# Performance work log

Hardware: AMD Instinct MI355X
Metric: run time of the kernel (lower is better)

## Reference

```python
import jax, jax.numpy as jnp
import numpy as np


def soft_threshold24(w):
    """2:4 soft thresholding along the last dim (groups of 4):
    keep top-2 magnitudes per group, subtract the 2nd-smallest magnitude
    (largest pruned value) from kept elements: sign(w)*relu(|w|-t)."""
    shape = w.shape
    g = w.reshape(-1, 4)
    mag = jnp.abs(g)
    s = jnp.sort(mag, axis=-1)          # ascending: [s0,s1,s2,s3]
    t = s[:, 1:2]                        # threshold = 2nd smallest magnitude
    out = jnp.sign(g) * jnp.maximum(mag - t, 0.0)
    return out.reshape(shape)


def fp8_mm(a, b):
    # fake_fp8_mm: cast operands to fp16, accumulate in fp32
    return jnp.matmul(a.astype(jnp.float16), b.astype(jnp.float16),
                      preferred_element_type=jnp.float32)


def _init_scale(w):
    ws = soft_threshold24(w)
    return jnp.sum(w * ws) / jnp.sum(ws * ws)


def setup_inputs() -> dict:
    key = jax.random.key(0)
    k1, k2, k3 = jax.random.split(key, 3)
    in_f, out_f, rank = 4096, 4096, 64
    B, S = 4, 2048
    x = jax.random.normal(k1, (B, S, in_f), dtype=jnp.float32)
    # kaiming_uniform_(a=sqrt(5)) -> U(-1/sqrt(fan_in), 1/sqrt(fan_in))
    b_in = 1.0 / np.sqrt(in_f)
    b_out = 1.0 / np.sqrt(rank)
    weight_in = jax.random.uniform(k2, (rank, in_f), minval=-b_in, maxval=b_in, dtype=jnp.float32)
    weight_out = jax.random.uniform(k3, (out_f, rank), minval=-b_out, maxval=b_out, dtype=jnp.float32)
    bias = jnp.zeros((out_f,), dtype=jnp.float32)
    scale_in = _init_scale(weight_in).astype(jnp.float32)
    scale_out = _init_scale(weight_out).astype(jnp.float32)
    return {"x": x, "weight_in": weight_in, "weight_out": weight_out,
            "bias": bias, "scale_in": scale_in, "scale_out": scale_out}


def reference(x, weight_in, weight_out, bias, scale_in, scale_out):
    rank = weight_in.shape[0]
    scaling = 1.0 / rank  # alpha / rank, alpha = 1.0
    sw_in = soft_threshold24(weight_in) * scale_in    # (rank, in_f)
    sw_out = soft_threshold24(weight_out) * scale_out  # (out_f, rank)
    B, S, in_f = x.shape
    xp = fp8_mm(x.reshape(-1, in_f), sw_in.T)          # (B*S, rank) fp32
    out = fp8_mm(xp, sw_out.T) + bias                   # (B*S, out_f)
    return out.reshape(B, S, -1) * scaling
```

## Files before the change

### kernel.cpp

```cpp
#include <hip/hip_runtime.h>

typedef _Float16 half8 __attribute__((ext_vector_type(8)));
typedef float f32x4 __attribute__((ext_vector_type(4)));

#define IN_F 4096
#define OUT_F 4096
#define RANK 64
#define M_TOT 8192
#define KCHUNK 1024
#define NKC (IN_F / KCHUNK)
#define KC2 512
#define NKC2 (IN_F / KC2)
#define NBLK (M_TOT / 16)

__device__ __forceinline__ half8 thresh8(const float* __restrict__ p, float scale) {
    half8 h;
    #pragma unroll
    for (int g = 0; g < 2; ++g) {
        f32x4 v = *(const f32x4*)(p + 4 * g);
        float m0 = fabsf(v[0]), m1 = fabsf(v[1]), m2 = fabsf(v[2]), m3 = fabsf(v[3]);
        float lo1 = fminf(m0, m1), hi1 = fmaxf(m0, m1);
        float lo2 = fminf(m2, m3), hi2 = fmaxf(m2, m3);
        float t = fminf(fmaxf(lo1, lo2), fminf(hi1, hi2));
        h[4 * g + 0] = (_Float16)(copysignf(fmaxf(m0 - t, 0.0f), v[0]) * scale);
        h[4 * g + 1] = (_Float16)(copysignf(fmaxf(m1 - t, 0.0f), v[1]) * scale);
        h[4 * g + 2] = (_Float16)(copysignf(fmaxf(m2 - t, 0.0f), v[2]) * scale);
        h[4 * g + 3] = (_Float16)(copysignf(fmaxf(m3 - t, 0.0f), v[3]) * scale);
    }
    return h;
}

__global__ __launch_bounds__(256) void prep_kernel(
    const float* __restrict__ w_in, const float* __restrict__ w_out,
    const float* __restrict__ s_in_p, const float* __restrict__ s_out_p,
    _Float16* __restrict__ sw_in, _Float16* __restrict__ sw_out)
{
    const int tid = blockIdx.x * 256 + threadIdx.x;
    const int HALF = RANK * IN_F / 8;
    const float* src; _Float16* dst; float sc; int g;
    if (tid < HALF) { src = w_in;  dst = sw_in;  sc = *s_in_p;  g = tid; }
    else            { src = w_out; dst = sw_out; sc = *s_out_p; g = tid - HALF; }
    half8 h = thresh8(src + (size_t)g * 8, sc);
    *(half8*)(dst + (size_t)g * 8) = h;
}

__global__ __launch_bounds__(256) void k_p1b(
    const float* __restrict__ x, const _Float16* __restrict__ sw_in,
    _Float16* __restrict__ xpw)
{
    __shared__ _Float16 xh[2][16][KC2];
    __shared__ _Float16 xpl[16][RANK];

    const int t    = threadIdx.x;
    const int wave = t >> 6;
    const int lane = t & 63;
    const int row  = lane & 15;
    const int kg   = lane >> 4;
    const int m0   = blockIdx.x * 16;
    const int sr   = wave;
    const int skb  = lane;

    f32x4 ra[4], rb[4];
    auto issue = [&](int kc) {
        #pragma unroll
        for (int i = 0; i < 4; ++i) {
            const float* src = x + (size_t)(m0 + i * 4 + sr) * IN_F + kc + skb * 8;
            ra[i] = *(const f32x4*)src;
            rb[i] = *(const f32x4*)(src + 4);
        }
    };
    auto cstore = [&](int buf) {
        #pragma unroll
        for (int i = 0; i < 4; ++i) {
            const int r = i * 4 + sr;
            half8 h;
            #pragma unroll
            for (int j = 0; j < 4; ++j) {
                h[j]     = (_Float16)ra[i][j];
                h[j + 4] = (_Float16)rb[i][j];
            }
            *(half8*)&xh[buf][r][(skb ^ (r & 7)) << 3] = h;
        }
    };

    const _Float16* wr = sw_in + (size_t)(wave * 16 + row) * IN_F + kg * 8;
    f32x4 acc1 = {0.f, 0.f, 0.f, 0.f};

    issue(0);
    cstore(0);
    __syncthreads();
    int cur = 0;
    #pragma unroll 1
    for (int kci = 0; kci < NKC2; ++kci) {
        if (kci + 1 < NKC2) issue((kci + 1) * KC2);
        const int kc = kci * KC2;
        #pragma unroll
        for (int k0 = 0; k0 < KC2; k0 += 64) {
            const int kb = (k0 >> 3) + kg;
            half8 alo = *(const half8*)&xh[cur][row][(kb       ^ (row & 7)) << 3];
            half8 ahi = *(const half8*)&xh[cur][row][((kb + 4) ^ (row & 7)) << 3];
            half8 blo = *(const half8*)(wr + kc + k0);
            half8 bhi = *(const half8*)(wr + kc + k0 + 32);
            acc1 = __builtin_amdgcn_mfma_f32_16x16x32_f16(alo, blo, acc1, 0, 0, 0);
            acc1 = __builtin_amdgcn_mfma_f32_16x16x32_f16(ahi, bhi, acc1, 0, 0, 0);
        }
        if (kci + 1 < NKC2) cstore(cur ^ 1);
        __syncthreads();
        cur ^= 1;
    }

    #pragma unroll
    for (int r = 0; r < 4; ++r)
        xpl[kg * 4 + r][wave * 16 + row] = (_Float16)acc1[r];
    __syncthreads();

    for (int i = t; i < 16 * RANK; i += 256)
        xpw[(size_t)blockIdx.x * 1024 + i] = xpl[i >> 6][i & 63];
}

__global__ __launch_bounds__(256) void k_p2(
    const _Float16* __restrict__ xpw, const _Float16* __restrict__ sw_out,
    const float* __restrict__ bias, float* __restrict__ out)
{
    __shared__ __align__(16) char smem[2 * 16 * KCHUNK * 2];
    __shared__ _Float16 xpl[16][RANK];

    const int t    = threadIdx.x;
    const int wave = t >> 6;
    const int lane = t & 63;
    const int row  = lane & 15;
    const int kg   = lane >> 4;
    const int m0   = blockIdx.x * 16;

    for (int i = t; i < 16 * RANK; i += 256)
        xpl[i >> 6][i & 63] = xpw[(size_t)blockIdx.x * 1024 + i];
    __syncthreads();

    const half8 a_lo = *(const half8*)&xpl[row][kg * 8];
    const half8 a_hi = *(const half8*)&xpl[row][kg * 8 + 32];
    const float scaling = 1.0f / 64.0f;

    float* tb = (float*)smem + wave * 2048;
    const int ncol0 = wave * 1024;

    for (int g = 0; g < 8; ++g) {
        const int gc = ncol0 + g * 128;
        #pragma unroll
        for (int c2 = 0; c2 < 2; ++c2) {
            const int cg = gc + c2 * 64;
            f32x4 acc[4] = {{0.f,0.f,0.f,0.f},{0.f,0.f,0.f,0.f},
                            {0.f,0.f,0.f,0.f},{0.f,0.f,0.f,0.f}};
            #pragma unroll
            for (int nt = 0; nt < 4; ++nt) {
                const _Float16* wp = sw_out + (size_t)(cg + nt * 16 + row) * RANK + kg * 8;
                half8 blo = *(const half8*)wp;
                half8 bhi = *(const half8*)(wp + 32);
                acc[nt] = __builtin_amdgcn_mfma_f32_16x16x32_f16(a_lo, blo, acc[nt], 0, 0, 0);
                acc[nt] = __builtin_amdgcn_mfma_f32_16x16x32_f16(a_hi, bhi, acc[nt], 0, 0, 0);
            }
            #pragma unroll
            for (int nt = 0; nt < 4; ++nt) {
                const float b = bias[cg + nt * 16 + row];
                #pragma unroll
                for (int r = 0; r < 4; ++r)
                    tb[(kg * 4 + r) * 128 + c2 * 64 + nt * 16 + row] =
                        (acc[nt][r] + b) * scaling;
            }
        }
        #pragma unroll
        for (int i = 0; i < 8; ++i) {
            const int s    = i * 64 + lane;
            const int orow = s >> 5;
            const int c4   = s & 31;
            f32x4 v = *(const f32x4*)&tb[orow * 128 + c4 * 4];
            *(f32x4*)&out[(size_t)(m0 + orow) * OUT_F + gc + c4 * 4] = v;
        }
    }
}

__global__ __launch_bounds__(256) void k_full(
    const float* __restrict__ x, const _Float16* __restrict__ sw_in,
    const _Float16* __restrict__ sw_out, const float* __restrict__ bias,
    float* __restrict__ out)
{
    __shared__ __align__(16) char smem[2 * 16 * KCHUNK * 2];
    __shared__ _Float16 xpl[16][RANK];
    auto xh = (_Float16 (*)[16][KCHUNK])smem;

    const int t    = threadIdx.x;
    const int wave = t >> 6;
    const int lane = t & 63;
    const int row  = lane & 15;
    const int kg   = lane >> 4;
    const int m0   = blockIdx.x * 16;
    const int sr   = t >> 7;
    const int skb  = t & 127;

    f32x4 ra[8], rb[8];
    auto issue = [&](int kc) {
        #pragma unroll
        for (int i = 0; i < 8; ++i) {
            const float* src = x + (size_t)(m0 + i * 2 + sr) * IN_F + kc + skb * 8;
            ra[i] = *(const f32x4*)src;
            rb[i] = *(const f32x4*)(src + 4);
        }
    };
    auto cstore = [&](int buf) {
        #pragma unroll
        for (int i = 0; i < 8; ++i) {
            const int r = i * 2 + sr;
            half8 h;
            #pragma unroll
            for (int j = 0; j < 4; ++j) {
                h[j]     = (_Float16)ra[i][j];
                h[j + 4] = (_Float16)rb[i][j];
            }
            *(half8*)&xh[buf][r][(skb ^ (r & 7)) << 3] = h;
        }
    };

    const _Float16* wr = sw_in + (size_t)(wave * 16 + row) * IN_F + kg * 8;
    f32x4 acc1 = {0.f, 0.f, 0.f, 0.f};

    issue(0);
    cstore(0);
    __syncthreads();
    int cur = 0;
    for (int kci = 0; kci < NKC; ++kci) {
        if (kci + 1 < NKC) issue((kci + 1) * KCHUNK);
        const int kc = kci * KCHUNK;
        #pragma unroll 4
        for (int k0 = 0; k0 < KCHUNK; k0 += 64) {
            const int kb = (k0 >> 3) + kg;
            half8 alo = *(const half8*)&xh[cur][row][(kb       ^ (row & 7)) << 3];
            half8 ahi = *(const half8*)&xh[cur][row][((kb + 4) ^ (row & 7)) << 3];
            half8 blo = *(const half8*)(wr + kc + k0);
            half8 bhi = *(const half8*)(wr + kc + k0 + 32);
            acc1 = __builtin_amdgcn_mfma_f32_16x16x32_f16(alo, blo, acc1, 0, 0, 0);
            acc1 = __builtin_amdgcn_mfma_f32_16x16x32_f16(ahi, bhi, acc1, 0, 0, 0);
        }
        if (kci + 1 < NKC) cstore(cur ^ 1);
        __syncthreads();
        cur ^= 1;
    }

    #pragma unroll
    for (int r = 0; r < 4; ++r)
        xpl[kg * 4 + r][wave * 16 + row] = (_Float16)acc1[r];
    __syncthreads();

    const half8 a_lo = *(const half8*)&xpl[row][kg * 8];
    const half8 a_hi = *(const half8*)&xpl[row][kg * 8 + 32];
    const float scaling = 1.0f / 64.0f;

    float* tb = (float*)smem + wave * 2048;
    const int ncol0 = wave * 1024;

    for (int g = 0; g < 8; ++g) {
        const int gc = ncol0 + g * 128;
        #pragma unroll
        for (int c2 = 0; c2 < 2; ++c2) {
            const int cg = gc + c2 * 64;
            f32x4 acc[4] = {{0.f,0.f,0.f,0.f},{0.f,0.f,0.f,0.f},
                            {0.f,0.f,0.f,0.f},{0.f,0.f,0.f,0.f}};
            #pragma unroll
            for (int nt = 0; nt < 4; ++nt) {
                const _Float16* wp = sw_out + (size_t)(cg + nt * 16 + row) * RANK + kg * 8;
                half8 blo = *(const half8*)wp;
                half8 bhi = *(const half8*)(wp + 32);
                acc[nt] = __builtin_amdgcn_mfma_f32_16x16x32_f16(a_lo, blo, acc[nt], 0, 0, 0);
                acc[nt] = __builtin_amdgcn_mfma_f32_16x16x32_f16(a_hi, bhi, acc[nt], 0, 0, 0);
            }
            #pragma unroll
            for (int nt = 0; nt < 4; ++nt) {
                const float b = bias[cg + nt * 16 + row];
                #pragma unroll
                for (int r = 0; r < 4; ++r)
                    tb[(kg * 4 + r) * 128 + c2 * 64 + nt * 16 + row] =
                        (acc[nt][r] + b) * scaling;
            }
        }
        #pragma unroll
        for (int i = 0; i < 8; ++i) {
            const int s    = i * 64 + lane;
            const int orow = s >> 5;
            const int c4   = s & 31;
            f32x4 v = *(const f32x4*)&tb[orow * 128 + c4 * 4];
            *(f32x4*)&out[(size_t)(m0 + orow) * OUT_F + gc + c4 * 4] = v;
        }
    }
}

__global__ __launch_bounds__(256) void loro_fallback(
    const float* __restrict__ x, const float* __restrict__ w_in,
    const float* __restrict__ w_out, const float* __restrict__ bias,
    const float* __restrict__ s_in_p, const float* __restrict__ s_out_p,
    float* __restrict__ out)
{
    __shared__ _Float16 xh[16][KCHUNK];
    __shared__ _Float16 xpl[16][RANK];

    const int t    = threadIdx.x;
    const int wave = t >> 6;
    const int lane = t & 63;
    const int row  = lane & 15;
    const int kg   = lane >> 4;
    const int m0   = blockIdx.x * 16;
    const float s_in  = *s_in_p;
    const float s_out = *s_out_p;

    f32x4 acc1 = {0.f, 0.f, 0.f, 0.f};
    const float* wr = w_in + (size_t)(wave * 16 + row) * IN_F + kg * 8;

    for (int kc = 0; kc < IN_F; kc += KCHUNK) {
        __syncthreads();
        #pragma unroll
        for (int i = 0; i < 8; ++i) {
            const int f  = i * 2048 + t * 8;
            const int r  = f >> 10;
            const int cl = f & (KCHUNK - 1);
            const float* src = x + (size_t)(m0 + r) * IN_F + kc + cl;
            f32x4 a = *(const f32x4*)src;
            f32x4 b = *(const f32x4*)(src + 4);
            #pragma unroll
            for (int j = 0; j < 4; ++j) {
                xh[r][cl + j]     = (_Float16)a[j];
                xh[r][cl + 4 + j] = (_Float16)b[j];
            }
        }
        __syncthreads();

        #pragma unroll 4
        for (int k0 = 0; k0 < KCHUNK; k0 += 64) {
            half8 alo = *(const half8*)&xh[row][k0 + kg * 8];
            half8 ahi = *(const half8*)&xh[row][k0 + kg * 8 + 32];
            half8 blo = thresh8(wr + kc + k0,      s_in);
            half8 bhi = thresh8(wr + kc + k0 + 32, s_in);
            acc1 = __builtin_amdgcn_mfma_f32_16x16x32_f16(alo, blo, acc1, 0, 0, 0);
            acc1 = __builtin_amdgcn_mfma_f32_16x16x32_f16(ahi, bhi, acc1, 0, 0, 0);
        }
    }

    #pragma unroll
    for (int r = 0; r < 4; ++r)
        xpl[kg * 4 + r][wave * 16 + row] = (_Float16)acc1[r];
    __syncthreads();

    const half8 a_lo = *(const half8*)&xpl[row][kg * 8];
    const half8 a_hi = *(const half8*)&xpl[row][kg * 8 + 32];
    const float scaling = 1.0f / 64.0f;

    for (int c = 0; c < 16; ++c) {
        f32x4 acc[4] = {{0.f,0.f,0.f,0.f},{0.f,0.f,0.f,0.f},
                        {0.f,0.f,0.f,0.f},{0.f,0.f,0.f,0.f}};
        #pragma unroll
        for (int nt = 0; nt < 4; ++nt) {
            const float* wp = w_out
                + (size_t)(c * 256 + wave * 64 + nt * 16 + row) * RANK + kg * 8;
            half8 blo = thresh8(wp,      s_out);
            half8 bhi = thresh8(wp + 32, s_out);
            acc[nt] = __builtin_amdgcn_mfma_f32_16x16x32_f16(a_lo, blo, acc[nt], 0, 0, 0);
            acc[nt] = __builtin_amdgcn_mfma_f32_16x16x32_f16(a_hi, bhi, acc[nt], 0, 0, 0);
        }
        #pragma unroll
        for (int nt = 0; nt < 4; ++nt) {
            const int col = c * 256 + wave * 64 + nt * 16 + row;
            const float b = bias[col];
            #pragma unroll
            for (int r = 0; r < 4; ++r)
                out[(size_t)(m0 + kg * 4 + r) * OUT_F + col] = (acc[nt][r] + b) * scaling;
        }
    }
}

extern "C" void kernel_launch(void* const* d_in, const int* in_sizes, int n_in,
                              void* d_out, int out_size, void* d_ws, size_t ws_size,
                              hipStream_t stream) {
    (void)in_sizes; (void)n_in; (void)out_size;
    const float* x     = (const float*)d_in[0];
    const float* w_in  = (const float*)d_in[1];
    const float* w_out = (const float*)d_in[2];
    const float* bias  = (const float*)d_in[3];
    const float* s_in  = (const float*)d_in[4];
    const float* s_out = (const float*)d_in[5];
    float* out = (float*)d_out;

    const size_t need_sw   = (size_t)(RANK * IN_F + OUT_F * RANK) * sizeof(_Float16);
    const size_t need_full = need_sw + (size_t)NBLK * 1024 * sizeof(_Float16);

    if (d_ws != nullptr && ws_size >= need_full) {
        _Float16* sw_in  = (_Float16*)d_ws;
        _Float16* sw_out = sw_in + (size_t)RANK * IN_F;
        _Float16* xpw    = (_Float16*)((char*)d_ws + need_sw);

        prep_kernel<<<(RANK * IN_F + OUT_F * RANK) / 8 / 256, 256, 0, stream>>>(
            w_in, w_out, s_in, s_out, sw_in, sw_out);
        k_p1b<<<NBLK, 256, 0, stream>>>(x, sw_in, xpw);
        k_p2 <<<NBLK, 256, 0, stream>>>(xpw, sw_out, bias, out);
    } else if (d_ws != nullptr && ws_size >= need_sw) {
        _Float16* sw_in  = (_Float16*)d_ws;
        _Float16* sw_out = sw_in + (size_t)RANK * IN_F;
        prep_kernel<<<(RANK * IN_F + OUT_F * RANK) / 8 / 256, 256, 0, stream>>>(
            w_in, w_out, s_in, s_out, sw_in, sw_out);
        k_full<<<NBLK, 256, 0, stream>>>(x, sw_in, sw_out, bias, out);
    } else {
        loro_fallback<<<M_TOT / 16, 256, 0, stream>>>(
            x, w_in, w_out, bias, s_in, s_out, out);
    }
}
```

Baseline: 103.1 us.

## Stage x via direct global-to-LDS loads and split K across two wave groups

Replaces the register-staged fp32-to-fp16 conversion of x in the first GEMM with direct global_load_lds transfers of raw fp32 into a swizzled LDS double buffer, converting to fp16 only when reading fragments. Block size grows to 512 threads, with two wave groups alternating K chunks and combining their partial results through an LDS reduction before writing xp. The aim is to hide global load latency without tying up registers and to give more waves per block for latency hiding. In exchange, LDS use doubles because data is stored as fp32, and half the waves sit idle in each chunk iteration.

```diff
diff --git a/kernel.cpp b/kernel.cpp
--- a/kernel.cpp
+++ b/kernel.cpp
@@ -9,8 +9,6 @@
 #define M_TOT 8192
 #define KCHUNK 1024
 #define NKC (IN_F / KCHUNK)
-#define KC2 512
-#define NKC2 (IN_F / KC2)
 #define NBLK (M_TOT / 16)
 
 __device__ __forceinline__ half8 thresh8(const float* __restrict__ p, float scale) {
@@ -44,78 +42,83 @@
     *(half8*)(dst + (size_t)g * 8) = h;
 }
 
-__global__ __launch_bounds__(256) void k_p1b(
+__global__ __launch_bounds__(512) void k_p1g(
     const float* __restrict__ x, const _Float16* __restrict__ sw_in,
     _Float16* __restrict__ xpw)
 {
-    __shared__ _Float16 xh[2][16][KC2];
-    __shared__ _Float16 xpl[16][RANK];
+    __shared__ float xf[2][16][512];
+    __shared__ float red[2][16][RANK];
 
     const int t    = threadIdx.x;
     const int wave = t >> 6;
     const int lane = t & 63;
     const int row  = lane & 15;
     const int kg   = lane >> 4;
+    const int kh   = wave >> 2;
+    const int ng   = wave & 3;
     const int m0   = blockIdx.x * 16;
-    const int sr   = wave;
-    const int skb  = lane;
-
-    f32x4 ra[4], rb[4];
-    auto issue = [&](int kc) {
-        #pragma unroll
-        for (int i = 0; i < 4; ++i) {
-            const float* src = x + (size_t)(m0 + i * 4 + sr) * IN_F + kc + skb * 8;
-            ra[i] = *(const f32x4*)src;
-            rb[i] = *(const f32x4*)(src + 4);
+    const int rs   = row & 7;
+
+    auto stage = [&](int buf, int kc) {
+        #pragma unroll
+        for (int j = 0; j < 4; ++j) {
+            const int s  = wave * 4 + j;
+            const int r  = s >> 1;
+            const int b  = (s & 1) * 64 + lane;
+            const int gb = b ^ (r & 7);
+            const float* g = x + (size_t)(m0 + r) * IN_F + kc + gb * 4;
+            void* l = (void*)&xf[buf][r][(s & 1) * 256];
+            __builtin_amdgcn_global_load_lds(
+                (const __attribute__((address_space(1))) void*)g,
+                (__attribute__((address_space(3))) void*)l, 16, 0, 0);
         }
     };
-    auto cstore = [&](int buf) {
-        #pragma unroll
-        for (int i = 0; i < 4; ++i) {
-            const int r = i * 4 + sr;
-            half8 h;
-            #pragma unroll
-            for (int j = 0; j < 4; ++j) {
-                h[j]     = (_Float16)ra[i][j];
-                h[j + 4] = (_Float16)rb[i][j];
-            }
-            *(half8*)&xh[buf][r][(skb ^ (r & 7)) << 3] = h;
-        }
-    };
-
-    const _Float16* wr = sw_in + (size_t)(wave * 16 + row) * IN_F + kg * 8;
+
+    const _Float16* wr = sw_in + (size_t)(ng * 16 + row) * IN_F + kg * 8;
     f32x4 acc1 = {0.f, 0.f, 0.f, 0.f};
 
-    issue(0);
-    cstore(0);
+    stage(0, 0);
     __syncthreads();
     int cur = 0;
     #pragma unroll 1
-    for (int kci = 0; kci < NKC2; ++kci) {
-        if (kci + 1 < NKC2) issue((kci + 1) * KC2);
-        const int kc = kci * KC2;
-        #pragma unroll
-        for (int k0 = 0; k0 < KC2; k0 += 64) {
-            const int kb = (k0 >> 3) + kg;
-            half8 alo = *(const half8*)&xh[cur][row][(kb       ^ (row & 7)) << 3];
-            half8 ahi = *(const half8*)&xh[cur][row][((kb + 4) ^ (row & 7)) << 3];
-            half8 blo = *(const half8*)(wr + kc + k0);
-            half8 bhi = *(const half8*)(wr + kc + k0 + 32);
-            acc1 = __builtin_amdgcn_mfma_f32_16x16x32_f16(alo, blo, acc1, 0, 0, 0);
-            acc1 = __builtin_amdgcn_mfma_f32_16x16x32_f16(ahi, bhi, acc1, 0, 0, 0);
-        }
-        if (kci + 1 < NKC2) cstore(cur ^ 1);
+    for (int kci = 0; kci < 8; ++kci) {
+        if (kci + 1 < 8) stage(cur ^ 1, (kci + 1) * 512);
+        if ((kci & 1) == kh) {
+            const int kc = kci * 512;
+            #pragma unroll
+            for (int k0 = 0; k0 < 512; k0 += 64) {
+                const int g0 = (k0 >> 2) + kg * 2;
+                const float* base = &xf[cur][row][0];
+                f32x4 a0 = *(const f32x4*)(base + (((g0    ) ^ rs) << 2));
+                f32x4 a1 = *(const f32x4*)(base + (((g0 + 1) ^ rs) << 2));
+                f32x4 a2 = *(const f32x4*)(base + (((g0 + 8) ^ rs) << 2));
+                f32x4 a3 = *(const f32x4*)(base + (((g0 + 9) ^ rs) << 2));
+                half8 alo, ahi;
+                #pragma unroll
+                for (int i = 0; i < 4; ++i) {
+                    alo[i]     = (_Float16)a0[i];
+                    alo[i + 4] = (_Float16)a1[i];
+                    ahi[i]     = (_Float16)a2[i];
+                    ahi[i + 4] = (_Float16)a3[i];
+                }
+                half8 blo = *(const half8*)(wr + kc + k0);
+                half8 bhi = *(const half8*)(wr + kc + k0 + 32);
+                acc1 = __builtin_amdgcn_mfma_f32_16x16x32_f16(alo, blo, acc1, 0, 0, 0);
+                acc1 = __builtin_amdgcn_mfma_f32_16x16x32_f16(ahi, bhi, acc1, 0, 0, 0);
+            }
+        }
         __syncthreads();
         cur ^= 1;
     }
 
     #pragma unroll
     for (int r = 0; r < 4; ++r)
-        xpl[kg * 4 + r][wave * 16 + row] = (_Float16)acc1[r];
-    __syncthreads();
-
-    for (int i = t; i < 16 * RANK; i += 256)
-        xpw[(size_t)blockIdx.x * 1024 + i] = xpl[i >> 6][i & 63];
+        red[kh][kg * 4 + r][ng * 16 + row] = acc1[r];
+    __syncthreads();
+
+    for (int i = t; i < 16 * RANK; i += 512)
+        xpw[(size_t)blockIdx.x * 1024 + i] =
+            (_Float16)(red[0][i >> 6][i & 63] + red[1][i >> 6][i & 63]);
 }
 
 __global__ __launch_bounds__(256) void k_p2(
@@ -395,7 +398,7 @@
 
         prep_kernel<<<(RANK * IN_F + OUT_F * RANK) / 8 / 256, 256, 0, stream>>>(
             w_in, w_out, s_in, s_out, sw_in, sw_out);
-        k_p1b<<<NBLK, 256, 0, stream>>>(x, sw_in, xpw);
+        k_p1g<<<NBLK, 512, 0, stream>>>(x, sw_in, xpw);
         k_p2 <<<NBLK, 256, 0, stream>>>(xpw, sw_out, bias, out);
     } else if (d_ws != nullptr && ws_size >= need_sw) {
         _Float16* sw_in  = (_Float16*)d_ws;
```

After: 106.9 us. 3.7% more time.
